# Optimization experiments

Hardware: AMD Instinct MI355X
Metric: run time of the kernel (lower is better)

## Reference

```python
import jax, jax.numpy as jnp
import numpy as np

HEADS = 16
D_MODEL = 1024
HEAD_DIM = D_MODEL // HEADS


def setup_inputs() -> dict:
    key = jax.random.key(0)
    ks = jax.random.split(key, 11)
    B, S, D = 2, 2048, D_MODEL
    s = 1.0 / np.sqrt(D)
    inp = {
        'Q': jax.random.normal(ks[0], (B, S, D), jnp.float32),
        'K': jax.random.normal(ks[1], (B, S, D), jnp.float32),
        'V': jax.random.normal(ks[2], (B, S, D), jnp.float32),
        'Wq': jax.random.normal(ks[3], (D, D), jnp.float32) * s,
        'Wk': jax.random.normal(ks[4], (D, D), jnp.float32) * s,
        'Wv': jax.random.normal(ks[5], (D, D), jnp.float32) * s,
        'Wo': jax.random.normal(ks[6], (D, D), jnp.float32) * s,
        'bq': jnp.zeros((D,), jnp.float32),
        'bk': jnp.zeros((D,), jnp.float32),
        'bv': jnp.zeros((D,), jnp.float32),
        'bo': jnp.zeros((D,), jnp.float32),
    }
    return inp


def reference(Q, K, V, Wq, Wk, Wv, Wo, bq, bk, bv, bo):
    B, S, D = Q.shape
    H, Dh = HEADS, HEAD_DIM
    # projections (torch Linear: x @ W.T + b)
    q = (Q @ Wq.T + bq).reshape(B, S, H, Dh).transpose(0, 2, 1, 3)  # [B,H,S,Dh]
    k = (K @ Wk.T + bk).reshape(B, S, H, Dh).transpose(0, 2, 1, 3)
    v = (V @ Wv.T + bv).reshape(B, S, H, Dh).transpose(0, 2, 1, 3)
    # naive scaled dot-product attention, scale = 1/sqrt(head_dim)
    scores = jnp.einsum('bhqd,bhkd->bhqk', q, k) / jnp.sqrt(jnp.float32(Dh))
    attn = jax.nn.softmax(scores, axis=-1)
    out = jnp.einsum('bhqk,bhkd->bhqd', attn, v)
    concat = out.transpose(0, 2, 1, 3).reshape(B, S, D)
    return concat @ Wo.T + bo
```

## Files before the change

kernel.cpp:

```cpp
#include <hip/hip_runtime.h>
#include <hip/hip_bf16.h>


#define SEQ     2048
#define DMODEL  1024
#define NHEADS  16
#define DH      64
#define MROWS   4096
#define M1      (1024*1024)
#define M4      (4*1024*1024)
#define SCQ     0.18033688f

typedef __hip_bfloat16 bf16;
typedef __attribute__((ext_vector_type(8))) short  short8;
typedef __attribute__((ext_vector_type(4))) float  f32x4;

__device__ __forceinline__ bf16 f2b(float x) { return __float2bfloat16(x); }
__device__ __forceinline__ float u2f(unsigned short u) {
    union { unsigned int i; float f; } x; x.i = ((unsigned int)u) << 16; return x.f;
}
__device__ __forceinline__ f32x4 mfma16(short8 a, short8 b, f32x4 c) {
    return __builtin_amdgcn_mfma_f32_16x16x32_bf16(a, b, c, 0, 0, 0);
}
__device__ __forceinline__ unsigned pk2(float a, float b) {
    union { __hip_bfloat162 h; unsigned u; } x;
    x.h = __float22bfloat162_rn(float2{a, b});
    return x.u;
}
__device__ __forceinline__ short8 pk8(float4 a, float4 b) {
    union { short8 s; unsigned u[4]; } x;
    x.u[0] = pk2(a.x, a.y); x.u[1] = pk2(a.z, a.w);
    x.u[2] = pk2(b.x, b.y); x.u[3] = pk2(b.z, b.w);
    return x.s;
}
__device__ __forceinline__ float fexp2(float x) {
    return __builtin_amdgcn_exp2f(x);
}
#define GLDS(g, l) __builtin_amdgcn_global_load_lds( \
    (const __attribute__((address_space(1))) void*)(g), \
    (__attribute__((address_space(3))) void*)(l), 16, 0, 0)

__global__ __launch_bounds__(256) void cvt_all(
    const float* __restrict__ Wq, const float* __restrict__ Wk,
    const float* __restrict__ Wv, const float* __restrict__ Wo,
    const float* __restrict__ Q,  const float* __restrict__ K,
    const float* __restrict__ V,  bf16* __restrict__ dst)
{
    const size_t gid = (size_t)blockIdx.x * 256 + threadIdx.x;
    const size_t e0 = gid * 8;
    const float* s;
    if (e0 < (size_t)4 * M1) {
        const float* w[4] = {Wq, Wk, Wv, Wo};
        s = w[e0 >> 20] + (e0 & (M1 - 1));
    } else {
        const float* a[4] = {nullptr, Q, K, V};
        s = a[e0 >> 22] + (e0 & (M4 - 1));
    }
    float4 x = *(const float4*)s, y = *(const float4*)(s + 4);
    *(short8*)((short*)dst + e0) = pk8(x, y);
}

__global__ __launch_bounds__(256) void cvt_w(
    const float* __restrict__ W0, const float* __restrict__ W1,
    const float* __restrict__ W2, const float* __restrict__ W3,
    bf16* __restrict__ dst)
{
    const int gid = blockIdx.x * 256 + threadIdx.x;
    const int t   = gid >> 17;
    const int off = (gid & 131071) * 8;
    const float* srcs[4] = {W0, W1, W2, W3};
    const float* s = srcs[t] + off;
    float4 a = *(const float4*)s, b = *(const float4*)(s + 4);
    *(short8*)((short*)dst + (size_t)gid * 8) = pk8(a, b);
}

__global__ __launch_bounds__(256) void cvt_1(
    const float* __restrict__ X, bf16* __restrict__ D)
{
    const int gid = blockIdx.x * 256 + threadIdx.x;
    const int off = gid * 8;
    float4 a = *(const float4*)(X + off), b = *(const float4*)(X + off + 4);
    *(short8*)((short*)D + off) = pk8(a, b);
}

template <int BN>
__device__ __forceinline__ void gemm_body(
    const bf16* __restrict__ A, const bf16* __restrict__ B,
    const float* __restrict__ bias, void* __restrict__ outp,
    int m0, int n0, int mode, int bias_m, float scale)
{
    __shared__ short As[128 * 32];
    __shared__ short Bs[BN * 32];
    constexpr int NI = BN / 32;

    const int tid  = threadIdx.x;
    const int lane = tid & 63;
    const int wv   = tid >> 6;
    const int wm   = (wv >> 1) * 64;
    const int wn   = (wv & 1) * (BN / 2);
    const int fn   = lane & 15;
    const int fq   = lane >> 4;

    const int srow = lane >> 2;
    const int scol = (lane & 3) * 8;

    const short* Ag = (const short*)A;
    const short* Bg = (const short*)B;

    f32x4 acc[4][NI];
#pragma unroll
    for (int i = 0; i < 4; ++i)
#pragma unroll
        for (int j = 0; j < NI; ++j) acc[i][j] = (f32x4){0.f, 0.f, 0.f, 0.f};

    for (int k0 = 0; k0 < DMODEL; k0 += 32) {
#pragma unroll
        for (int i = 0; i < 2; ++i) {
            const int rr = wv * 32 + i * 16;
            const short* ga = Ag + (size_t)(m0 + rr + srow) * DMODEL + k0 + scol;
            GLDS(ga, As + rr * 32);
        }
#pragma unroll
        for (int i = 0; i < BN / 64; ++i) {
            const int rr = wv * (BN / 4) + i * 16;
            const short* gb = Bg + (size_t)(n0 + rr + srow) * DMODEL + k0 + scol;
            GLDS(gb, Bs + rr * 32);
        }
        __syncthreads();

        short8 af[4], bfr[NI];
#pragma unroll
        for (int im = 0; im < 4; ++im)
            af[im] = *(const short8*)(As + (wm + im * 16 + fn) * 32 + fq * 8);
#pragma unroll
        for (int in = 0; in < NI; ++in)
            bfr[in] = *(const short8*)(Bs + (wn + in * 16 + fn) * 32 + fq * 8);
#pragma unroll
        for (int im = 0; im < 4; ++im)
#pragma unroll
            for (int in = 0; in < NI; ++in)
                acc[im][in] = mfma16(af[im], bfr[in], acc[im][in]);
        __syncthreads();
    }

#pragma unroll
    for (int im = 0; im < 4; ++im) {
#pragma unroll
        for (int in = 0; in < NI; ++in) {
#pragma unroll
            for (int r = 0; r < 4; ++r) {
                const int m = m0 + wm + im * 16 + fq * 4 + r;
                const int n = n0 + wn + in * 16 + fn;
                const float c = (acc[im][in][r] + (bias_m ? bias[m] : bias[n])) * scale;
                if (mode == 0) {
                    ((float*)outp)[(size_t)m * DMODEL + n] = c;
                } else if (mode == 1) {
                    const int b = m >> 11, s = m & (SEQ - 1);
                    const int h = n >> 6,  d = n & (DH - 1);
                    ((bf16*)outp)[(((size_t)(b * NHEADS + h) * SEQ) + s) * DH + d] = f2b(c);
                } else {
                    const int h = m >> 6,  d = m & (DH - 1);
                    const int b = n >> 11, s = n & (SEQ - 1);
                    const int p = s & 31;
                    const int sp = (s & ~31) | ((p & 12) << 1) | ((p & 16) >> 2) | (p & 3);
                    ((bf16*)outp)[(((size_t)(b * NHEADS + h) * DH) + d) * SEQ + sp] = f2b(c);
                }
            }
        }
    }
}

__global__ __launch_bounds__(256, 3) void gemm_one(
    const bf16* A, const bf16* B, const float* bias, void* out,
    int mode, int bias_m, float scale)
{
    gemm_body<128>(A, B, bias, out, blockIdx.x * 128, blockIdx.y * 128,
                   mode, bias_m, scale);
}

__global__ __launch_bounds__(256, 3) void gemm_fin(
    const bf16* A, const bf16* B, const float* bias, void* out)
{
    gemm_body<64>(A, B, bias, out, blockIdx.x * 128, blockIdx.y * 64, 0, 0, 1.f);
}

__global__ __launch_bounds__(256, 3) void gemm_qkv(
    const bf16* Qb, const bf16* Kb, const bf16* Vb, const bf16* Wb,
    const float* bq, const float* bk, const float* bv,
    bf16* qp, bf16* kp, bf16* vp)
{
    const int blk = blockIdx.x;
    const int z = blk >> 8, t = blk & 255;
    if (z == 0)
        gemm_body<128>(Qb, Wb,          bq, qp, (t >> 3) * 128, (t & 7) * 128, 1, 0, SCQ);
    else if (z == 1)
        gemm_body<128>(Kb, Wb + M1,     bk, kp, (t >> 3) * 128, (t & 7) * 128, 1, 0, 1.f);
    else
        gemm_body<128>(Wb + 2 * M1, Vb, bv, vp, (t >> 5) * 128, (t & 31) * 128, 2, 1, 1.f);
}

struct AttnState {
    f32x4 O[4][2];
    f32x4 lacc[2];
};

__global__ __launch_bounds__(256, 4) void attn_part(
    const bf16* __restrict__ q,
    const bf16* __restrict__ k,
    const bf16* __restrict__ vt,
    bf16* __restrict__ Op0, bf16* __restrict__ Op1,
    float* __restrict__ lscr)
{
    __shared__ short Kt[2][64 * 64];
    __shared__ short Vt[2][64 * 64];

    const int tid  = threadIdx.x;
    const int wave = tid >> 6;
    const int lane = tid & 63;
    const int n    = lane & 15;
    const int quad = lane >> 4;

    const int blk  = blockIdx.x;
    const int xcd  = blk & 7;
    const int rest = blk >> 3;
    const int qt   = rest & 15;
    const int kh   = (rest >> 4) & 1;
    const int bh   = ((rest >> 5) << 3) | xcd;
    const int q0w  = qt * 128 + wave * 32;
    const int kt0  = kh * 16;

    const bf16* qhead = q  + (size_t)bh * SEQ * DH;
    const bf16* khead = k  + (size_t)bh * SEQ * DH;
    const bf16* vhead = vt + (size_t)bh * DH * SEQ;

    short8 qf[2][2];
#pragma unroll
    for (int qg = 0; qg < 2; ++qg) {
        const short* qr = (const short*)(qhead + (size_t)(q0w + qg * 16 + n) * DH);
        qf[qg][0] = *(const short8*)(qr + quad * 8);
        qf[qg][1] = *(const short8*)(qr + 32 + quad * 8);
    }

    const short8 onesv = {(short)0x3F80, (short)0x3F80, (short)0x3F80, (short)0x3F80,
                          (short)0x3F80, (short)0x3F80, (short)0x3F80, (short)0x3F80};
    const f32x4 Zv = (f32x4){0.f, 0.f, 0.f, 0.f};

    f32x4 O[4][2];
#pragma unroll
    for (int gd = 0; gd < 4; ++gd)
#pragma unroll
        for (int qg = 0; qg < 2; ++qg) O[gd][qg] = Zv;
    f32x4 lacc[2] = {Zv, Zv};

    const int srow = lane >> 3;
    const int schk = (lane & 7) ^ srow;
    const int off0 = ((quad       ^ (n & 7)) * 8);
    const int off1 = (((4 + quad) ^ (n & 7)) * 8);

    auto stage = [&](int kt, int buf) {
        const int kbase = kt * 64;
#pragma unroll
        for (int i = 0; i < 2; ++i) {
            const int r = wave * 16 + i * 8 + srow;
            const char* gk = (const char*)(khead + (size_t)(kbase + r) * DH) + schk * 16;
            const char* gv = (const char*)(vhead + (size_t)r * SEQ + kbase) + schk * 16;
            GLDS(gk, Kt[buf] + (wave * 16 + i * 8) * 64);
            GLDS(gv, Vt[buf] + (wave * 16 + i * 8) * 64);
        }
    };

    auto tile_body = [&](const short* KtB, const short* VtB) {
        f32x4 st[4][2];
#pragma unroll
        for (int g = 0; g < 4; ++g) {
            const short* kr = KtB + (g * 16 + n) * 64;
            short8 kf0 = *(const short8*)(kr + off0);
            short8 kf1 = *(const short8*)(kr + off1);
#pragma unroll
            for (int qg = 0; qg < 2; ++qg) {
                f32x4 s = mfma16(kf0, qf[qg][0], Zv);
                s = mfma16(kf1, qf[qg][1], s);
                st[g][qg] = s;
            }
        }
        short8 bP[2][2];
#pragma unroll
        for (int t = 0; t < 2; ++t) {
#pragma unroll
            for (int qg = 0; qg < 2; ++qg) {
                union { short8 s8; unsigned u[4]; } bb;
                bb.u[0] = pk2(fexp2(st[2*t][qg][0]),   fexp2(st[2*t][qg][1]));
                bb.u[1] = pk2(fexp2(st[2*t][qg][2]),   fexp2(st[2*t][qg][3]));
                bb.u[2] = pk2(fexp2(st[2*t+1][qg][0]), fexp2(st[2*t+1][qg][1]));
                bb.u[3] = pk2(fexp2(st[2*t+1][qg][2]), fexp2(st[2*t+1][qg][3]));
                bP[t][qg] = bb.s8;
                lacc[qg] = mfma16(onesv, bP[t][qg], lacc[qg]);
            }
        }
#pragma unroll
        for (int gd = 0; gd < 4; ++gd) {
            const short* vr = VtB + (gd * 16 + n) * 64;
            short8 vf0 = *(const short8*)(vr + off0);
            short8 vf1 = *(const short8*)(vr + off1);
#pragma unroll
            for (int qg = 0; qg < 2; ++qg) {
                O[gd][qg] = mfma16(vf0, bP[0][qg], O[gd][qg]);
                O[gd][qg] = mfma16(vf1, bP[1][qg], O[gd][qg]);
            }
        }
    };

    stage(kt0, 0);
#pragma unroll 1
    for (int t = 0; t < 16; t += 2) {
        __syncthreads();
        stage(kt0 + t + 1, 1);
        tile_body(Kt[0], Vt[0]);
        __syncthreads();
        if (t + 2 < 16) stage(kt0 + t + 2, 0);
        tile_body(Kt[1], Vt[1]);
    }

    const int b = bh >> 4;
    const int h = bh & (NHEADS - 1);
    bf16* Op = kh ? Op1 : Op0;
#pragma unroll
    for (int gd = 0; gd < 4; ++gd) {
#pragma unroll
        for (int qg = 0; qg < 2; ++qg) {
            const int s = q0w + qg * 16 + n;
            uint2 o;
            o.x = pk2(O[gd][qg][0], O[gd][qg][1]);
            o.y = pk2(O[gd][qg][2], O[gd][qg][3]);
            *(uint2*)(Op + ((size_t)(b * SEQ + s)) * DMODEL + h * DH + gd * 16 + quad * 4) = o;
        }
    }
    if (quad == 0) {
#pragma unroll
        for (int qg = 0; qg < 2; ++qg)
            lscr[kh * (MROWS * NHEADS / 1) / 1 * 0 + kh * 65536
                 + (b * NHEADS + h) * SEQ + q0w + qg * 16 + n] = lacc[qg][0];
    }
}

__global__ __launch_bounds__(256) void attn_merge(
    const bf16* __restrict__ Op0, const bf16* __restrict__ Op1,
    const float* __restrict__ lscr, bf16* __restrict__ ao)
{
    const int gid = blockIdx.x * 256 + threadIdx.x;
    const int e = gid * 8;
    const int row = e >> 10;
    const int col = e & 1023;
    const int b = row >> 11, s = row & (SEQ - 1), h = col >> 6;
    const int li = (b * NHEADS + h) * SEQ + s;
    const float inv = 1.0f / (lscr[li] + lscr[65536 + li]);

    union { short8 s8; unsigned short us[8]; } a, c;
    a.s8 = *(const short8*)((const short*)Op0 + e);
    c.s8 = *(const short8*)((const short*)Op1 + e);
    float f[8];
#pragma unroll
    for (int i = 0; i < 8; ++i) f[i] = (u2f(a.us[i]) + u2f(c.us[i])) * inv;
    uint4 o;
    o.x = pk2(f[0], f[1]); o.y = pk2(f[2], f[3]);
    o.z = pk2(f[4], f[5]); o.w = pk2(f[6], f[7]);
    *(uint4*)((short*)ao + e) = o;
}

__global__ __launch_bounds__(256) void attn_mfma(
    const bf16* __restrict__ q,
    const bf16* __restrict__ k,
    const bf16* __restrict__ vt,
    bf16* __restrict__ out)
{
    __shared__ short Kt[2][64 * 64];
    __shared__ short Vt[2][64 * 64];

    const int tid  = threadIdx.x;
    const int wave = tid >> 6;
    const int lane = tid & 63;
    const int n    = lane & 15;
    const int quad = lane >> 4;

    const int blk  = blockIdx.x;
    const int xcd  = blk & 7;
    const int rest = blk >> 3;
    const int qt   = rest & 15;
    const int bh   = ((rest >> 4) << 3) | xcd;
    const int q0w  = qt * 128 + wave * 32;

    const bf16* qhead = q  + (size_t)bh * SEQ * DH;
    const bf16* khead = k  + (size_t)bh * SEQ * DH;
    const bf16* vhead = vt + (size_t)bh * DH * SEQ;

    short8 qf[2][2];
#pragma unroll
    for (int qg = 0; qg < 2; ++qg) {
        const short* qr = (const short*)(qhead + (size_t)(q0w + qg * 16 + n) * DH);
        qf[qg][0] = *(const short8*)(qr + quad * 8);
        qf[qg][1] = *(const short8*)(qr + 32 + quad * 8);
    }

    const short8 onesv = {(short)0x3F80, (short)0x3F80, (short)0x3F80, (short)0x3F80,
                          (short)0x3F80, (short)0x3F80, (short)0x3F80, (short)0x3F80};
    const f32x4 Zv = (f32x4){0.f, 0.f, 0.f, 0.f};

    f32x4 O[4][2];
#pragma unroll
    for (int gd = 0; gd < 4; ++gd)
#pragma unroll
        for (int qg = 0; qg < 2; ++qg) O[gd][qg] = Zv;
    f32x4 lacc[2] = {Zv, Zv};

    const int srow = lane >> 3;
    const int schk = (lane & 7) ^ srow;
    const int off0 = ((quad       ^ (n & 7)) * 8);
    const int off1 = (((4 + quad) ^ (n & 7)) * 8);

    auto stage = [&](int kt, int buf) {
        const int kbase = kt * 64;
#pragma unroll
        for (int i = 0; i < 2; ++i) {
            const int r = wave * 16 + i * 8 + srow;
            const char* gk = (const char*)(khead + (size_t)(kbase + r) * DH) + schk * 16;
            const char* gv = (const char*)(vhead + (size_t)r * SEQ + kbase) + schk * 16;
            GLDS(gk, Kt[buf] + (wave * 16 + i * 8) * 64);
            GLDS(gv, Vt[buf] + (wave * 16 + i * 8) * 64);
        }
    };

    auto tile_body = [&](const short* KtB, const short* VtB) {
        f32x4 st[4][2];
#pragma unroll
        for (int g = 0; g < 4; ++g) {
            const short* kr = KtB + (g * 16 + n) * 64;
            short8 kf0 = *(const short8*)(kr + off0);
            short8 kf1 = *(const short8*)(kr + off1);
#pragma unroll
            for (int qg = 0; qg < 2; ++qg) {
                f32x4 s = mfma16(kf0, qf[qg][0], Zv);
                s = mfma16(kf1, qf[qg][1], s);
                st[g][qg] = s;
            }
        }
        short8 bP[2][2];
#pragma unroll
        for (int t = 0; t < 2; ++t) {
#pragma unroll
            for (int qg = 0; qg < 2; ++qg) {
                union { short8 s8; unsigned u[4]; } bb;
                bb.u[0] = pk2(fexp2(st[2*t][qg][0]),   fexp2(st[2*t][qg][1]));
                bb.u[1] = pk2(fexp2(st[2*t][qg][2]),   fexp2(st[2*t][qg][3]));
                bb.u[2] = pk2(fexp2(st[2*t+1][qg][0]), fexp2(st[2*t+1][qg][1]));
                bb.u[3] = pk2(fexp2(st[2*t+1][qg][2]), fexp2(st[2*t+1][qg][3]));
                bP[t][qg] = bb.s8;
                lacc[qg] = mfma16(onesv, bP[t][qg], lacc[qg]);
            }
        }
#pragma unroll
        for (int gd = 0; gd < 4; ++gd) {
            const short* vr = VtB + (gd * 16 + n) * 64;
            short8 vf0 = *(const short8*)(vr + off0);
            short8 vf1 = *(const short8*)(vr + off1);
#pragma unroll
            for (int qg = 0; qg < 2; ++qg) {
                O[gd][qg] = mfma16(vf0, bP[0][qg], O[gd][qg]);
                O[gd][qg] = mfma16(vf1, bP[1][qg], O[gd][qg]);
            }
        }
    };

    stage(0, 0);
#pragma unroll 1
    for (int kt = 0; kt < SEQ / 64; kt += 2) {
        __syncthreads();
        stage(kt + 1, 1);
        tile_body(Kt[0], Vt[0]);
        __syncthreads();
        if (kt + 2 < SEQ / 64) stage(kt + 2, 0);
        tile_body(Kt[1], Vt[1]);
    }

    const float inv0 = 1.0f / lacc[0][0];
    const float inv1 = 1.0f / lacc[1][0];
    const int b = bh >> 4;
    const int h = bh & (NHEADS - 1);
#pragma unroll
    for (int gd = 0; gd < 4; ++gd) {
#pragma unroll
        for (int qg = 0; qg < 2; ++qg) {
            const float iv = qg ? inv1 : inv0;
            const int s = q0w + qg * 16 + n;
            uint2 o;
            o.x = pk2(O[gd][qg][0] * iv, O[gd][qg][1] * iv);
            o.y = pk2(O[gd][qg][2] * iv, O[gd][qg][3] * iv);
            *(uint2*)(out + ((size_t)(b * SEQ + s)) * DMODEL + h * DH + gd * 16 + quad * 4) = o;
        }
    }
}

extern "C" void kernel_launch(void* const* d_in, const int* in_sizes, int n_in,
                              void* d_out, int out_size, void* d_ws, size_t ws_size,
                              hipStream_t stream) {
    const float* Q  = (const float*)d_in[0];
    const float* K  = (const float*)d_in[1];
    const float* V  = (const float*)d_in[2];
    const float* Wq = (const float*)d_in[3];
    const float* Wk = (const float*)d_in[4];
    const float* Wv = (const float*)d_in[5];
    const float* Wo = (const float*)d_in[6];
    const float* bq = (const float*)d_in[7];
    const float* bk = (const float*)d_in[8];
    const float* bv = (const float*)d_in[9];
    const float* bo = (const float*)d_in[10];

    bf16* kp = (bf16*)d_out;
    bf16* vp = kp + M4;

    dim3 bb(256);
    dim3 gqk(MROWS / 128, DMODEL / 128);
    dim3 gvv(DMODEL / 128, MROWS / 128);
    dim3 gfin(MROWS / 128, DMODEL / 64);

    if (ws_size >= (size_t)40 * 1024 * 1024) {
        bf16* Wb = (bf16*)d_ws;
        bf16* Qb = Wb + 4 * M1;
        bf16* Kb = Qb + M4;
        bf16* Vb = Kb + M4;
        bf16* qp = Vb + M4;
        bf16* ao = Qb;

        cvt_all<<<8192, bb, 0, stream>>>(Wq, Wk, Wv, Wo, Q, K, V, Wb);
        gemm_qkv<<<768, bb, 0, stream>>>(Qb, Kb, Vb, Wb, bq, bk, bv, qp, kp, vp);
        attn_part<<<1024, bb, 0, stream>>>(qp, kp, vp, Kb, Vb, (float*)Wb);
        attn_merge<<<2048, bb, 0, stream>>>(Kb, Vb, (const float*)Wb, ao);
        gemm_fin<<<gfin, bb, 0, stream>>>(ao, Wb + 3 * M1, bo, d_out);
    } else {
        bf16* Wb = (bf16*)d_ws;
        bf16* Xb = Wb + 4 * M1;
        bf16* qp = Xb + M4;
        bf16* ao = Xb;

        cvt_w<<<2048, bb, 0, stream>>>(Wq, Wk, Wv, Wo, Wb);
        cvt_1<<<2048, bb, 0, stream>>>(Q, Xb);
        gemm_one<<<gqk, bb, 0, stream>>>(Xb, Wb, bq, qp, 1, 0, SCQ);
        cvt_1<<<2048, bb, 0, stream>>>(K, Xb);
        gemm_one<<<gqk, bb, 0, stream>>>(Xb, Wb + M1, bk, kp, 1, 0, 1.f);
        cvt_1<<<2048, bb, 0, stream>>>(V, Xb);
        gemm_one<<<gvv, bb, 0, stream>>>(Wb + 2 * M1, Xb, bv, vp, 2, 1, 1.f);
        attn_mfma<<<512, bb, 0, stream>>>(qp, kp, vp, ao);
        gemm_fin<<<gfin, bb, 0, stream>>>(ao, Wb + 3 * M1, bo, d_out);
    }
}
```

Measured before the change: 216.6 us.

## Fuse split-K attention halves into one block with LDS-based merge

Replaces the two-kernel split-key attention (partial kernel writing bf16 partial outputs plus row sums, then a merge kernel) with a single 512-thread block in which two groups of four waves each process half of the key range. The halves are then combined through shared memory and the normalized result is written directly. This removes the global round trip of the partial outputs and sums as well as one kernel launch, and it keeps the partials in fp32 instead of rounding them to bf16. In exchange each block uses more LDS and twice the threads, which can lower how many blocks fit per CU, and it adds an extra barrier and merge phase at the end.

Result: faster. 210.1 us (-3.0%).

```diff
diff --git a/kernel.cpp b/kernel.cpp
--- a/kernel.cpp
+++ b/kernel.cpp
@@ -199,23 +199,18 @@
         gemm_body<128>(Wb + 2 * M1, Vb, bv, vp, (t >> 5) * 128, (t & 31) * 128, 2, 1, 1.f);
 }
 
-struct AttnState {
-    f32x4 O[4][2];
-    f32x4 lacc[2];
-};
-
-__global__ __launch_bounds__(256, 4) void attn_part(
+__global__ __launch_bounds__(512, 4) void attn_fused(
     const bf16* __restrict__ q,
     const bf16* __restrict__ k,
     const bf16* __restrict__ vt,
-    bf16* __restrict__ Op0, bf16* __restrict__ Op1,
-    float* __restrict__ lscr)
-{
-    __shared__ short Kt[2][64 * 64];
-    __shared__ short Vt[2][64 * 64];
+    bf16* __restrict__ out)
+{
+    __shared__ short LB[32768];
 
     const int tid  = threadIdx.x;
     const int wave = tid >> 6;
+    const int half = wave >> 2;
+    const int w4   = wave & 3;
     const int lane = tid & 63;
     const int n    = lane & 15;
     const int quad = lane >> 4;
@@ -224,14 +219,16 @@
     const int xcd  = blk & 7;
     const int rest = blk >> 3;
     const int qt   = rest & 15;
-    const int kh   = (rest >> 4) & 1;
-    const int bh   = ((rest >> 5) << 3) | xcd;
-    const int q0w  = qt * 128 + wave * 32;
-    const int kt0  = kh * 16;
+    const int bh   = ((rest >> 4) << 3) | xcd;
+    const int q0w  = qt * 128 + w4 * 32;
+    const int kt0  = half * 16;
 
     const bf16* qhead = q  + (size_t)bh * SEQ * DH;
     const bf16* khead = k  + (size_t)bh * SEQ * DH;
     const bf16* vhead = vt + (size_t)bh * DH * SEQ;
+
+    short* Kb0 = LB + half * 16384;
+    short* Vb0 = LB + half * 16384 + 8192;
 
     short8 qf[2][2];
 #pragma unroll
@@ -250,7 +247,7 @@
     for (int gd = 0; gd < 4; ++gd)
 #pragma unroll
         for (int qg = 0; qg < 2; ++qg) O[gd][qg] = Zv;
-    f32x4 lacc[2] = {Zv, Zv};
+    f32x4 lacc[2][2] = {{Zv, Zv}, {Zv, Zv}};
 
     const int srow = lane >> 3;
     const int schk = (lane & 7) ^ srow;
@@ -261,11 +258,11 @@
         const int kbase = kt * 64;
 #pragma unroll
         for (int i = 0; i < 2; ++i) {
-            const int r = wave * 16 + i * 8 + srow;
+            const int r = w4 * 16 + i * 8 + srow;
             const char* gk = (const char*)(khead + (size_t)(kbase + r) * DH) + schk * 16;
             const char* gv = (const char*)(vhead + (size_t)r * SEQ + kbase) + schk * 16;
-            GLDS(gk, Kt[buf] + (wave * 16 + i * 8) * 64);
-            GLDS(gv, Vt[buf] + (wave * 16 + i * 8) * 64);
+            GLDS(gk, Kb0 + buf * 4096 + (w4 * 16 + i * 8) * 64);
+            GLDS(gv, Vb0 + buf * 4096 + (w4 * 16 + i * 8) * 64);
         }
     };
 
@@ -294,7 +291,7 @@
                 bb.u[2] = pk2(fexp2(st[2*t+1][qg][0]), fexp2(st[2*t+1][qg][1]));
                 bb.u[3] = pk2(fexp2(st[2*t+1][qg][2]), fexp2(st[2*t+1][qg][3]));
                 bP[t][qg] = bb.s8;
-                lacc[qg] = mfma16(onesv, bP[t][qg], lacc[qg]);
+                lacc[t][qg] = mfma16(onesv, bP[t][qg], lacc[t][qg]);
             }
         }
 #pragma unroll
@@ -315,56 +312,49 @@
     for (int t = 0; t < 16; t += 2) {
         __syncthreads();
         stage(kt0 + t + 1, 1);
-        tile_body(Kt[0], Vt[0]);
+        tile_body(Kb0, Vb0);
         __syncthreads();
         if (t + 2 < 16) stage(kt0 + t + 2, 0);
-        tile_body(Kt[1], Vt[1]);
-    }
-
-    const int b = bh >> 4;
-    const int h = bh & (NHEADS - 1);
-    bf16* Op = kh ? Op1 : Op0;
-#pragma unroll
-    for (int gd = 0; gd < 4; ++gd) {
-#pragma unroll
-        for (int qg = 0; qg < 2; ++qg) {
-            const int s = q0w + qg * 16 + n;
-            uint2 o;
-            o.x = pk2(O[gd][qg][0], O[gd][qg][1]);
-            o.y = pk2(O[gd][qg][2], O[gd][qg][3]);
-            *(uint2*)(Op + ((size_t)(b * SEQ + s)) * DMODEL + h * DH + gd * 16 + quad * 4) = o;
-        }
-    }
-    if (quad == 0) {
-#pragma unroll
-        for (int qg = 0; qg < 2; ++qg)
-            lscr[kh * (MROWS * NHEADS / 1) / 1 * 0 + kh * 65536
-                 + (b * NHEADS + h) * SEQ + q0w + qg * 16 + n] = lacc[qg][0];
-    }
-}
-
-__global__ __launch_bounds__(256) void attn_merge(
-    const bf16* __restrict__ Op0, const bf16* __restrict__ Op1,
-    const float* __restrict__ lscr, bf16* __restrict__ ao)
-{
-    const int gid = blockIdx.x * 256 + threadIdx.x;
-    const int e = gid * 8;
-    const int row = e >> 10;
-    const int col = e & 1023;
-    const int b = row >> 11, s = row & (SEQ - 1), h = col >> 6;
-    const int li = (b * NHEADS + h) * SEQ + s;
-    const float inv = 1.0f / (lscr[li] + lscr[65536 + li]);
-
-    union { short8 s8; unsigned short us[8]; } a, c;
-    a.s8 = *(const short8*)((const short*)Op0 + e);
-    c.s8 = *(const short8*)((const short*)Op1 + e);
-    float f[8];
-#pragma unroll
-    for (int i = 0; i < 8; ++i) f[i] = (u2f(a.us[i]) + u2f(c.us[i])) * inv;
-    uint4 o;
-    o.x = pk2(f[0], f[1]); o.y = pk2(f[2], f[3]);
-    o.z = pk2(f[4], f[5]); o.w = pk2(f[6], f[7]);
-    *(uint4*)((short*)ao + e) = o;
+        tile_body(Kb0 + 4096, Vb0 + 4096);
+    }
+
+    float* scr = (float*)LB + (size_t)(w4 * 64 + lane) * 34;
+    const float l0 = lacc[0][0][0] + lacc[1][0][0];
+    const float l1 = lacc[0][1][0] + lacc[1][1][0];
+
+    __syncthreads();
+    if (half == 1) {
+#pragma unroll
+        for (int gd = 0; gd < 4; ++gd)
+#pragma unroll
+            for (int qg = 0; qg < 2; ++qg) {
+                *(float2*)(scr + (gd * 2 + qg) * 4)     = float2{O[gd][qg][0], O[gd][qg][1]};
+                *(float2*)(scr + (gd * 2 + qg) * 4 + 2) = float2{O[gd][qg][2], O[gd][qg][3]};
+            }
+        *(float2*)(scr + 32) = float2{l0, l1};
+    }
+    __syncthreads();
+    if (half == 0) {
+        const float2 lo = *(const float2*)(scr + 32);
+        const float inv0 = 1.0f / (l0 + lo.x);
+        const float inv1 = 1.0f / (l1 + lo.y);
+        const int b = bh >> 4;
+        const int h = bh & (NHEADS - 1);
+#pragma unroll
+        for (int gd = 0; gd < 4; ++gd) {
+#pragma unroll
+            for (int qg = 0; qg < 2; ++qg) {
+                const float iv = qg ? inv1 : inv0;
+                float2 a = *(const float2*)(scr + (gd * 2 + qg) * 4);
+                float2 c = *(const float2*)(scr + (gd * 2 + qg) * 4 + 2);
+                const int s = q0w + qg * 16 + n;
+                uint2 o;
+                o.x = pk2((O[gd][qg][0] + a.x) * iv, (O[gd][qg][1] + a.y) * iv);
+                o.y = pk2((O[gd][qg][2] + c.x) * iv, (O[gd][qg][3] + c.y) * iv);
+                *(uint2*)(out + ((size_t)(b * SEQ + s)) * DMODEL + h * DH + gd * 16 + quad * 4) = o;
+            }
+        }
+    }
 }
 
 __global__ __launch_bounds__(256) void attn_mfma(
@@ -532,8 +522,7 @@
 
         cvt_all<<<8192, bb, 0, stream>>>(Wq, Wk, Wv, Wo, Q, K, V, Wb);
         gemm_qkv<<<768, bb, 0, stream>>>(Qb, Kb, Vb, Wb, bq, bk, bv, qp, kp, vp);
-        attn_part<<<1024, bb, 0, stream>>>(qp, kp, vp, Kb, Vb, (float*)Wb);
-        attn_merge<<<2048, bb, 0, stream>>>(Kb, Vb, (const float*)Wb, ao);
+        attn_fused<<<512, 512, 0, stream>>>(qp, kp, vp, ao);
         gemm_fin<<<gfin, bb, 0, stream>>>(ao, Wb + 3 * M1, bo, d_out);
     } else {
         bf16* Wb = (bf16*)d_ws;
```
